# Performance work log

Hardware: AMD Instinct MI355X
Metric: run time of the kernel (lower is better)

The kernel has to match this reference:

```python
import jax, jax.numpy as jnp
import numpy as np

B, TO, C, T = 16, 8, 64, 1024


def setup_inputs() -> dict:
    key = jax.random.key(0)
    kx, kq, kk, kv, ko = jax.random.split(key, 5)
    s = 0.1
    return {
        "x": jax.random.normal(kx, (B, TO, C, T), dtype=jnp.float32),
        "Wq": jax.random.normal(kq, (C, C), dtype=jnp.float32) * s,
        "Wk": jax.random.normal(kk, (C, C), dtype=jnp.float32) * s,
        "Wv": jax.random.normal(kv, (C, C), dtype=jnp.float32) * s,
        "Wo": jax.random.normal(ko, (C, C), dtype=jnp.float32) * s,
        "scale": jnp.float32(1.0 / np.sqrt(C)),
    }


def reference(x, Wq, Wk, Wv, Wo, scale):
    b, to, c, t = x.shape
    xr = x.reshape(b * to, c, t)            # [N, C, T]
    # 1x1 conv1d (no bias) == channel-mixing matmul with weight [out_c, in_c]
    q = jnp.einsum('oc,bct->bot', Wq, xr)
    k = jnp.einsum('oc,bct->bot', Wk, xr)
    v = jnp.einsum('oc,bct->bot', Wv, xr)
    # attention over the time axis: scores [N, T, T]
    scores = jnp.einsum('bct,bcs->bts', q, k) * scale
    w = jax.nn.softmax(scores, axis=-1)
    out = jnp.einsum('bts,bcs->bct', w, v)  # [N, C, T]
    out = jnp.einsum('oc,bct->bot', Wo, out)
    out = out + xr
    return out.reshape(b, to, c, t)
```

## Files before the change

kernel.cpp:

```cpp
#include <hip/hip_runtime.h>
#include <hip/hip_bf16.h>

typedef __hip_bfloat16 bf16;
typedef __attribute__((ext_vector_type(8))) short short8;
typedef __attribute__((ext_vector_type(4))) short short4v;
typedef __attribute__((ext_vector_type(4))) float f32x4;
typedef __attribute__((ext_vector_type(4))) unsigned uint4v;

#define NB 128
#define CC 64
#define TT 1024

#if __has_builtin(__builtin_amdgcn_exp2f)
#define EXP2(x) __builtin_amdgcn_exp2f(x)
#else
#define EXP2(x) exp2f(x)
#endif

__device__ __forceinline__ unsigned rnd_u(float f) {
  return __builtin_bit_cast(unsigned, f) + 0x8000u;
}
__device__ __forceinline__ short f2bfs_fast(float f) {
  return (short)(rnd_u(f) >> 16);
}
__device__ __forceinline__ unsigned packbf2(unsigned uhi, unsigned ulo) {
  return __builtin_amdgcn_perm(uhi, ulo, 0x07060302);
}
__device__ __forceinline__ short4v pack4(float a, float b, float c, float d) {
  unsigned pd[2] = { packbf2(rnd_u(b), rnd_u(a)), packbf2(rnd_u(d), rnd_u(c)) };
  return *(const short4v*)pd;
}

__device__ __forceinline__ f32x4 mfma32(short8 a, short8 b, f32x4 c) {
  return __builtin_amdgcn_mfma_f32_16x16x32_bf16(a, b, c, 0, 0, 0);
}

__global__ __launch_bounds__(256) void wcvt(
    const float* __restrict__ Wq, const float* __restrict__ Wk,
    const float* __restrict__ Wv, const float* __restrict__ Wo,
    const float* __restrict__ scale_p, bf16* __restrict__ wb)
{
  const int i = blockIdx.x * 256 + threadIdx.x;
  float f;
  if      (i <  4096) f = Wq[i] * (*scale_p) * 1.44269504089f;
  else if (i <  8192) f = Wk[i - 4096];
  else if (i < 12288) f = Wv[i - 8192];
  else {
    const int ii = i - 12288;
    const int o  = ii >> 6;
    const int cp = ii & 63;
    const int u  = cp >> 5, q4 = (cp >> 3) & 3, j = cp & 7;
    const int c  = (2 * u + (j >> 2)) * 16 + q4 * 4 + (j & 3);
    f = Wo[o * 64 + c];
  }
  wb[i] = __float2bfloat16(f);
}

__global__ __launch_bounds__(256) void qkv_mfma(
    const float* __restrict__ x, const bf16* __restrict__ wb,
    bf16* __restrict__ qt, bf16* __restrict__ kt, bf16* __restrict__ v)
{
  __shared__ short xs[64 * 72];
  __shared__ short ys[64 * 72];

  const int n  = blockIdx.y;
  const int t0 = blockIdx.x * 64;
  const int tid = threadIdx.x;
  const int w  = tid >> 6, il = tid & 15, q4 = (tid & 63) >> 4;
  const size_t nbase = (size_t)n * (CC * TT);

  {
    const int tc = tid & 15;
    const int c0 = (tid >> 4) * 4;
    float fe[4][4];
    #pragma unroll
    for (int j = 0; j < 4; j++) {
      float4 fj = *(const float4*)&x[nbase + (size_t)(c0 + j) * TT + t0 + tc * 4];
      fe[j][0] = fj.x; fe[j][1] = fj.y; fe[j][2] = fj.z; fe[j][3] = fj.w;
    }
    #pragma unroll
    for (int e = 0; e < 4; e++)
      *(short4v*)&xs[(tc * 4 + e) * 72 + c0] = pack4(fe[0][e], fe[1][e], fe[2][e], fe[3][e]);
  }
  __syncthreads();

  short8 xa[2];
  #pragma unroll
  for (int kk = 0; kk < 2; kk++)
    xa[kk] = *(const short8*)&xs[(w * 16 + il) * 72 + kk * 32 + q4 * 8];

  const bf16* wq = wb;
  const bf16* wk = wb + 4096;
  const bf16* wv = wb + 8192;

  f32x4 aq[4], ak[4], av[4];
  #pragma unroll
  for (int i = 0; i < 4; i++) {
    aq[i] = (f32x4){0.f,0.f,0.f,0.f};
    ak[i] = (f32x4){0.f,0.f,0.f,0.f};
    av[i] = (f32x4){0.f,0.f,0.f,0.f};
  }

  #pragma unroll
  for (int kk = 0; kk < 2; kk++) {
    #pragma unroll
    for (int ot = 0; ot < 4; ot++) {
      const int ridx = (ot * 16 + il) * 64 + kk * 32 + q4 * 8;
      short8 bq = *(const short8*)&wq[ridx];
      short8 bk = *(const short8*)&wk[ridx];
      short8 bv = *(const short8*)&wv[ridx];
      aq[ot] = mfma32(xa[kk], bq, aq[ot]);
      ak[ot] = mfma32(xa[kk], bk, ak[ot]);
      av[ot] = mfma32(bv, xa[kk], av[ot]);
    }
  }

  const int rr = tid >> 2;
  const int sg = (tid & 3) * 8;

  __syncthreads();
  #pragma unroll
  for (int ot = 0; ot < 4; ot++)
    #pragma unroll
    for (int r = 0; r < 4; r++)
      ys[(w * 16 + q4 * 4 + r) * 72 + ot * 16 + il] = f2bfs_fast(aq[ot][r]);
  __syncthreads();
  *(short8*)&qt[nbase + (size_t)(t0 + rr) * 64 + sg]      = *(const short8*)&ys[rr * 72 + sg];
  *(short8*)&qt[nbase + (size_t)(t0 + rr) * 64 + sg + 32] = *(const short8*)&ys[rr * 72 + sg + 32];

  __syncthreads();
  #pragma unroll
  for (int ot = 0; ot < 4; ot++)
    #pragma unroll
    for (int r = 0; r < 4; r++)
      ys[(w * 16 + q4 * 4 + r) * 72 + ot * 16 + il] = f2bfs_fast(ak[ot][r]);
  __syncthreads();
  *(short8*)&kt[nbase + (size_t)(t0 + rr) * 64 + sg]      = *(const short8*)&ys[rr * 72 + sg];
  *(short8*)&kt[nbase + (size_t)(t0 + rr) * 64 + sg + 32] = *(const short8*)&ys[rr * 72 + sg + 32];

  __syncthreads();
  #pragma unroll
  for (int ot = 0; ot < 4; ot++)
    #pragma unroll
    for (int r = 0; r < 4; r++)
      ys[(ot * 16 + q4 * 4 + r) * 72 + (il >> 2) * 16 + w * 4 + (il & 3)] =
          f2bfs_fast(av[ot][r]);
  __syncthreads();
  *(short8*)&v[nbase + (size_t)rr * TT + t0 + sg]      = *(const short8*)&ys[rr * 72 + sg];
  *(short8*)&v[nbase + (size_t)rr * TT + t0 + sg + 32] = *(const short8*)&ys[rr * 72 + sg + 32];
}

__global__ __launch_bounds__(256, 4) void attn_flash(
    const bf16* __restrict__ qt, const bf16* __restrict__ kt,
    const bf16* __restrict__ v,  const bf16* __restrict__ wob,
    const float* __restrict__ x, float* __restrict__ out)
{
  __shared__ float obuf[64 * 132];
  short* ks = (short*)obuf;
  short* vs = ks + 64 * 72;

  const int bid = blockIdx.x;
  const int n   = bid & 127;
  const int qt0 = (bid >> 7) * 128;
  const int tid = threadIdx.x;
  const int w   = tid >> 6;
  const int il  = tid & 15;
  const int q4  = (tid & 63) >> 4;
  const size_t nbase = (size_t)n * (CC * TT);

  const int srow0 = tid >> 3, scol = (tid & 7) * 8;
  const int srow1 = srow0 + 32;

  short8 qb[2][2];
  #pragma unroll
  for (int mt = 0; mt < 2; mt++)
    #pragma unroll
    for (int kk = 0; kk < 2; kk++)
      qb[mt][kk] = *(const short8*)&qt[nbase +
          (size_t)(qt0 + w * 32 + mt * 16 + il) * 64 + kk * 32 + q4 * 8];

  const short8 ones8 = { 0x3F80, 0x3F80, 0x3F80, 0x3F80,
                         0x3F80, 0x3F80, 0x3F80, 0x3F80 };

  f32x4 oaccT[2][4];
  f32x4 lacc[2];
  #pragma unroll
  for (int mt = 0; mt < 2; mt++) {
    lacc[mt] = (f32x4){0.f, 0.f, 0.f, 0.f};
    #pragma unroll
    for (int ct = 0; ct < 4; ct++) oaccT[mt][ct] = (f32x4){0.f, 0.f, 0.f, 0.f};
  }

  short8 kreg0 = *(const short8*)&kt[nbase + (size_t)srow0 * 64 + scol];
  short8 kreg1 = *(const short8*)&kt[nbase + (size_t)srow1 * 64 + scol];
  short8 vreg0 = *(const short8*)&v[nbase + (size_t)srow0 * TT + scol];
  short8 vreg1 = *(const short8*)&v[nbase + (size_t)srow1 * TT + scol];

  #pragma unroll 1
  for (int st = 0; st < 16; st++) {
    __syncthreads();
    *(short8*)&ks[srow0 * 72 + scol] = kreg0;
    *(short8*)&ks[srow1 * 72 + scol] = kreg1;
    *(short8*)&vs[srow0 * 72 + scol] = vreg0;
    *(short8*)&vs[srow1 * 72 + scol] = vreg1;
    if (st < 15) {
      const int s1 = (st + 1) * 64;
      kreg0 = *(const short8*)&kt[nbase + (size_t)(s1 + srow0) * 64 + scol];
      kreg1 = *(const short8*)&kt[nbase + (size_t)(s1 + srow1) * 64 + scol];
      vreg0 = *(const short8*)&v[nbase + (size_t)srow0 * TT + s1 + scol];
      vreg1 = *(const short8*)&v[nbase + (size_t)srow1 * TT + s1 + scol];
    }
    __syncthreads();

    uint4v pq[2][2];
    #pragma unroll
    for (int st2 = 0; st2 < 4; st2++) {
      short8 ka0 = *(const short8*)&ks[(st2 * 16 + il) * 72 + q4 * 8];
      short8 ka1 = *(const short8*)&ks[(st2 * 16 + il) * 72 + 32 + q4 * 8];
      #pragma unroll
      for (int mt = 0; mt < 2; mt++) {
        f32x4 sT = (f32x4){0.f, 0.f, 0.f, 0.f};
        sT = mfma32(ka0, qb[mt][0], sT);
        sT = mfma32(ka1, qb[mt][1], sT);
        float p0 = EXP2(sT[0]), p1 = EXP2(sT[1]), p2 = EXP2(sT[2]), p3 = EXP2(sT[3]);
        pq[mt][st2 >> 1][(st2 & 1) * 2]     = packbf2(rnd_u(p1), rnd_u(p0));
        pq[mt][st2 >> 1][(st2 & 1) * 2 + 1] = packbf2(rnd_u(p3), rnd_u(p2));
      }
    }
    short8 pb[2][2];
    #pragma unroll
    for (int mt = 0; mt < 2; mt++)
      #pragma unroll
      for (int u = 0; u < 2; u++) {
        pb[mt][u] = __builtin_bit_cast(short8, pq[mt][u]);
        lacc[mt] = mfma32(ones8, pb[mt][u], lacc[mt]);
      }

    #pragma unroll
    for (int ct = 0; ct < 4; ct++) {
      short8 h0 = *(const short8*)&vs[(ct * 16 + il) * 72 + q4 * 16];
      short8 h1 = *(const short8*)&vs[(ct * 16 + il) * 72 + q4 * 16 + 8];
      #pragma unroll
      for (int mt = 0; mt < 2; mt++) {
        oaccT[mt][ct] = mfma32(h0, pb[mt][0], oaccT[mt][ct]);
        oaccT[mt][ct] = mfma32(h1, pb[mt][1], oaccT[mt][ct]);
      }
    }
  }

  float linv[2];
  #pragma unroll
  for (int mt = 0; mt < 2; mt++) linv[mt] = 1.f / lacc[mt][0];

  uint4v obq[2][2];
  #pragma unroll
  for (int mt = 0; mt < 2; mt++)
    #pragma unroll
    for (int ct = 0; ct < 4; ct++) {
      float a = oaccT[mt][ct][0] * linv[mt], b = oaccT[mt][ct][1] * linv[mt];
      float c = oaccT[mt][ct][2] * linv[mt], d = oaccT[mt][ct][3] * linv[mt];
      obq[mt][ct >> 1][(ct & 1) * 2]     = packbf2(rnd_u(b), rnd_u(a));
      obq[mt][ct >> 1][(ct & 1) * 2 + 1] = packbf2(rnd_u(d), rnd_u(c));
    }
  short8 ob8[2][2];
  #pragma unroll
  for (int mt = 0; mt < 2; mt++)
    #pragma unroll
    for (int u = 0; u < 2; u++)
      ob8[mt][u] = __builtin_bit_cast(short8, obq[mt][u]);

  __syncthreads();

  #pragma unroll
  for (int ot = 0; ot < 4; ot++) {
    short8 wa0 = *(const short8*)&wob[(ot * 16 + il) * 64 + q4 * 8];
    short8 wa1 = *(const short8*)&wob[(ot * 16 + il) * 64 + 32 + q4 * 8];
    #pragma unroll
    for (int mt = 0; mt < 2; mt++) {
      f32x4 res = (f32x4){0.f, 0.f, 0.f, 0.f};
      res = mfma32(wa0, ob8[mt][0], res);
      res = mfma32(wa1, ob8[mt][1], res);
      #pragma unroll
      for (int r = 0; r < 4; r++)
        obuf[(ot * 16 + q4 * 4 + r) * 132 + w * 32 + mt * 16 + il] = res[r];
    }
  }
  __syncthreads();

  const int orow = tid >> 3;
  const int ocb  = (tid & 7) * 4;
  #pragma unroll
  for (int half = 0; half < 2; half++) {
    const int row = orow + half * 32;
    #pragma unroll
    for (int k = 0; k < 4; k++) {
      const int col = ocb + k * 32;
      float4 val = *(const float4*)&obuf[row * 132 + col];
      const size_t idx = nbase + (size_t)row * TT + qt0 + col;
      float4 xv = *(const float4*)&x[idx];
      val.x += xv.x; val.y += xv.y; val.z += xv.z; val.w += xv.w;
      *(float4*)&out[idx] = val;
    }
  }
}

extern "C" void kernel_launch(void* const* d_in, const int* in_sizes, int n_in,
                              void* d_out, int out_size, void* d_ws, size_t ws_size,
                              hipStream_t stream) {
  const float* x     = (const float*)d_in[0];
  const float* Wq    = (const float*)d_in[1];
  const float* Wk    = (const float*)d_in[2];
  const float* Wv    = (const float*)d_in[3];
  const float* Wo    = (const float*)d_in[4];
  const float* scale = (const float*)d_in[5];
  float* out = (float*)d_out;

  const size_t elems = (size_t)NB * CC * TT;
  bf16* wb  = (bf16*)d_ws;
  bf16* qtb = wb + 16384;
  bf16* ktb = qtb + elems;
  bf16* vv  = ktb + elems;

  wcvt<<<64, 256, 0, stream>>>(Wq, Wk, Wv, Wo, scale, wb);
  qkv_mfma<<<dim3(TT / 64, NB), 256, 0, stream>>>(x, wb, qtb, ktb, vv);
  attn_flash<<<dim3(NB * (TT / 128)), 256, 0, stream>>>(qtb, ktb, vv, wb + 12288, x, out);
}
```

Measured before the change: 158.3 us.

## Fold Wq/Wk and Wo/Wv products and attend directly on x

Precomputes M = Wk^T Wq (with scale and log2e folded in) and W2 = Wo Wv on device, so scores become x^T M x and the output projection absorbs V. The attention kernel now loads fp32 x tiles for keys and values and converts them to bf16 in registers. This removes the QKV projection kernel and its bf16 Q/K/V round trip through global memory. The cost is reading fp32 x (twice the bytes of bf16) for every key/value tile in each block, plus bf16 rounding of the fused weight matrices.

```diff
diff --git a/kernel.cpp b/kernel.cpp
--- a/kernel.cpp
+++ b/kernel.cpp
@@ -20,9 +20,6 @@
 __device__ __forceinline__ unsigned rnd_u(float f) {
   return __builtin_bit_cast(unsigned, f) + 0x8000u;
 }
-__device__ __forceinline__ short f2bfs_fast(float f) {
-  return (short)(rnd_u(f) >> 16);
-}
 __device__ __forceinline__ unsigned packbf2(unsigned uhi, unsigned ulo) {
   return __builtin_amdgcn_perm(uhi, ulo, 0x07060302);
 }
@@ -35,127 +32,36 @@
   return __builtin_amdgcn_mfma_f32_16x16x32_bf16(a, b, c, 0, 0, 0);
 }
 
-__global__ __launch_bounds__(256) void wcvt(
+__global__ __launch_bounds__(256) void wprep(
     const float* __restrict__ Wq, const float* __restrict__ Wk,
     const float* __restrict__ Wv, const float* __restrict__ Wo,
-    const float* __restrict__ scale_p, bf16* __restrict__ wb)
+    const float* __restrict__ scale_p, bf16* __restrict__ wmw)
 {
-  const int i = blockIdx.x * 256 + threadIdx.x;
-  float f;
-  if      (i <  4096) f = Wq[i] * (*scale_p) * 1.44269504089f;
-  else if (i <  8192) f = Wk[i - 4096];
-  else if (i < 12288) f = Wv[i - 8192];
-  else {
-    const int ii = i - 12288;
-    const int o  = ii >> 6;
-    const int cp = ii & 63;
-    const int u  = cp >> 5, q4 = (cp >> 3) & 3, j = cp & 7;
-    const int c  = (2 * u + (j >> 2)) * 16 + q4 * 4 + (j & 3);
-    f = Wo[o * 64 + c];
-  }
-  wb[i] = __float2bfloat16(f);
-}
-
-__global__ __launch_bounds__(256) void qkv_mfma(
-    const float* __restrict__ x, const bf16* __restrict__ wb,
-    bf16* __restrict__ qt, bf16* __restrict__ kt, bf16* __restrict__ v)
-{
-  __shared__ short xs[64 * 72];
-  __shared__ short ys[64 * 72];
-
-  const int n  = blockIdx.y;
-  const int t0 = blockIdx.x * 64;
-  const int tid = threadIdx.x;
-  const int w  = tid >> 6, il = tid & 15, q4 = (tid & 63) >> 4;
-  const size_t nbase = (size_t)n * (CC * TT);
-
-  {
-    const int tc = tid & 15;
-    const int c0 = (tid >> 4) * 4;
-    float fe[4][4];
-    #pragma unroll
-    for (int j = 0; j < 4; j++) {
-      float4 fj = *(const float4*)&x[nbase + (size_t)(c0 + j) * TT + t0 + tc * 4];
-      fe[j][0] = fj.x; fe[j][1] = fj.y; fe[j][2] = fj.z; fe[j][3] = fj.w;
-    }
-    #pragma unroll
-    for (int e = 0; e < 4; e++)
-      *(short4v*)&xs[(tc * 4 + e) * 72 + c0] = pack4(fe[0][e], fe[1][e], fe[2][e], fe[3][e]);
-  }
-  __syncthreads();
-
-  short8 xa[2];
-  #pragma unroll
-  for (int kk = 0; kk < 2; kk++)
-    xa[kk] = *(const short8*)&xs[(w * 16 + il) * 72 + kk * 32 + q4 * 8];
-
-  const bf16* wq = wb;
-  const bf16* wk = wb + 4096;
-  const bf16* wv = wb + 8192;
-
-  f32x4 aq[4], ak[4], av[4];
-  #pragma unroll
-  for (int i = 0; i < 4; i++) {
-    aq[i] = (f32x4){0.f,0.f,0.f,0.f};
-    ak[i] = (f32x4){0.f,0.f,0.f,0.f};
-    av[i] = (f32x4){0.f,0.f,0.f,0.f};
-  }
-
-  #pragma unroll
-  for (int kk = 0; kk < 2; kk++) {
-    #pragma unroll
-    for (int ot = 0; ot < 4; ot++) {
-      const int ridx = (ot * 16 + il) * 64 + kk * 32 + q4 * 8;
-      short8 bq = *(const short8*)&wq[ridx];
-      short8 bk = *(const short8*)&wk[ridx];
-      short8 bv = *(const short8*)&wv[ridx];
-      aq[ot] = mfma32(xa[kk], bq, aq[ot]);
-      ak[ot] = mfma32(xa[kk], bk, ak[ot]);
-      av[ot] = mfma32(bv, xa[kk], av[ot]);
-    }
-  }
-
-  const int rr = tid >> 2;
-  const int sg = (tid & 3) * 8;
-
-  __syncthreads();
-  #pragma unroll
-  for (int ot = 0; ot < 4; ot++)
-    #pragma unroll
-    for (int r = 0; r < 4; r++)
-      ys[(w * 16 + q4 * 4 + r) * 72 + ot * 16 + il] = f2bfs_fast(aq[ot][r]);
-  __syncthreads();
-  *(short8*)&qt[nbase + (size_t)(t0 + rr) * 64 + sg]      = *(const short8*)&ys[rr * 72 + sg];
-  *(short8*)&qt[nbase + (size_t)(t0 + rr) * 64 + sg + 32] = *(const short8*)&ys[rr * 72 + sg + 32];
-
-  __syncthreads();
-  #pragma unroll
-  for (int ot = 0; ot < 4; ot++)
-    #pragma unroll
-    for (int r = 0; r < 4; r++)
-      ys[(w * 16 + q4 * 4 + r) * 72 + ot * 16 + il] = f2bfs_fast(ak[ot][r]);
-  __syncthreads();
-  *(short8*)&kt[nbase + (size_t)(t0 + rr) * 64 + sg]      = *(const short8*)&ys[rr * 72 + sg];
-  *(short8*)&kt[nbase + (size_t)(t0 + rr) * 64 + sg + 32] = *(const short8*)&ys[rr * 72 + sg + 32];
-
-  __syncthreads();
-  #pragma unroll
-  for (int ot = 0; ot < 4; ot++)
-    #pragma unroll
-    for (int r = 0; r < 4; r++)
-      ys[(ot * 16 + q4 * 4 + r) * 72 + (il >> 2) * 16 + w * 4 + (il & 3)] =
-          f2bfs_fast(av[ot][r]);
-  __syncthreads();
-  *(short8*)&v[nbase + (size_t)rr * TT + t0 + sg]      = *(const short8*)&ys[rr * 72 + sg];
-  *(short8*)&v[nbase + (size_t)rr * TT + t0 + sg + 32] = *(const short8*)&ys[rr * 72 + sg + 32];
-}
-
-__global__ __launch_bounds__(256, 4) void attn_flash(
-    const bf16* __restrict__ qt, const bf16* __restrict__ kt,
-    const bf16* __restrict__ v,  const bf16* __restrict__ wob,
+  const int g = blockIdx.x * 256 + threadIdx.x;
+  float acc = 0.f;
+  if (g < 4096) {
+    const int a = g >> 6, b = g & 63;
+    #pragma unroll 8
+    for (int c = 0; c < 64; c++) acc += Wk[c * 64 + a] * Wq[c * 64 + b];
+    acc *= (*scale_p) * 1.44269504089f;
+    wmw[g] = __float2bfloat16(acc);
+  } else {
+    const int ii = g - 4096;
+    const int o = ii >> 6, cp = ii & 63;
+    const int u = cp >> 5, q4 = (cp >> 3) & 3, j = cp & 7;
+    const int a = (2 * u + (j >> 2)) * 16 + q4 * 4 + (j & 3);
+    #pragma unroll 8
+    for (int c = 0; c < 64; c++) acc += Wo[o * 64 + c] * Wv[c * 64 + a];
+    wmw[g] = __float2bfloat16(acc);
+  }
+}
+
+__global__ __launch_bounds__(256, 4) void attn_fused(
+    const bf16* __restrict__ wm, const bf16* __restrict__ w2,
     const float* __restrict__ x, float* __restrict__ out)
 {
   __shared__ float obuf[64 * 132];
+  short* xq = (short*)obuf;
   short* ks = (short*)obuf;
   short* vs = ks + 64 * 72;
 
@@ -168,16 +74,54 @@
   const int q4  = (tid & 63) >> 4;
   const size_t nbase = (size_t)n * (CC * TT);
 
-  const int srow0 = tid >> 3, scol = (tid & 7) * 8;
-  const int srow1 = srow0 + 32;
-
-  short8 qb[2][2];
+  const int tc = tid & 15;
+  const int c0 = (tid >> 4) * 4;
+
+  #pragma unroll
+  for (int half = 0; half < 2; half++) {
+    float fe[4][4];
+    #pragma unroll
+    for (int j = 0; j < 4; j++) {
+      float4 fj = *(const float4*)&x[nbase + (size_t)(c0 + j) * TT + qt0 + half * 64 + tc * 4];
+      fe[j][0] = fj.x; fe[j][1] = fj.y; fe[j][2] = fj.z; fe[j][3] = fj.w;
+    }
+    #pragma unroll
+    for (int e = 0; e < 4; e++)
+      *(short4v*)&xq[(half * 64 + tc * 4 + e) * 72 + c0] =
+          pack4(fe[0][e], fe[1][e], fe[2][e], fe[3][e]);
+  }
+  __syncthreads();
+
+  f32x4 yacc[4][2];
+  #pragma unroll
+  for (int at = 0; at < 4; at++)
+    #pragma unroll
+    for (int mt = 0; mt < 2; mt++) yacc[at][mt] = (f32x4){0.f, 0.f, 0.f, 0.f};
+  #pragma unroll
+  for (int kk = 0; kk < 2; kk++) {
+    short8 xb0 = *(const short8*)&xq[(w * 32 + il) * 72 + kk * 32 + q4 * 8];
+    short8 xb1 = *(const short8*)&xq[(w * 32 + 16 + il) * 72 + kk * 32 + q4 * 8];
+    #pragma unroll
+    for (int at = 0; at < 4; at++) {
+      short8 ma = *(const short8*)&wm[(at * 16 + il) * 64 + kk * 32 + q4 * 8];
+      yacc[at][0] = mfma32(ma, xb0, yacc[at][0]);
+      yacc[at][1] = mfma32(ma, xb1, yacc[at][1]);
+    }
+  }
+  __syncthreads();
+  #pragma unroll
+  for (int at = 0; at < 4; at++)
+    #pragma unroll
+    for (int mt = 0; mt < 2; mt++)
+      *(short4v*)&xq[(w * 32 + mt * 16 + il) * 72 + at * 16 + q4 * 4] =
+          pack4(yacc[at][mt][0], yacc[at][mt][1], yacc[at][mt][2], yacc[at][mt][3]);
+  __syncthreads();
+  short8 yb[2][2];
   #pragma unroll
   for (int mt = 0; mt < 2; mt++)
     #pragma unroll
     for (int kk = 0; kk < 2; kk++)
-      qb[mt][kk] = *(const short8*)&qt[nbase +
-          (size_t)(qt0 + w * 32 + mt * 16 + il) * 64 + kk * 32 + q4 * 8];
+      yb[mt][kk] = *(const short8*)&xq[(w * 32 + mt * 16 + il) * 72 + kk * 32 + q4 * 8];
 
   const short8 ones8 = { 0x3F80, 0x3F80, 0x3F80, 0x3F80,
                          0x3F80, 0x3F80, 0x3F80, 0x3F80 };
@@ -191,24 +135,30 @@
     for (int ct = 0; ct < 4; ct++) oaccT[mt][ct] = (f32x4){0.f, 0.f, 0.f, 0.f};
   }
 
-  short8 kreg0 = *(const short8*)&kt[nbase + (size_t)srow0 * 64 + scol];
-  short8 kreg1 = *(const short8*)&kt[nbase + (size_t)srow1 * 64 + scol];
-  short8 vreg0 = *(const short8*)&v[nbase + (size_t)srow0 * TT + scol];
-  short8 vreg1 = *(const short8*)&v[nbase + (size_t)srow1 * TT + scol];
+  float fe[4][4];
+  #pragma unroll
+  for (int j = 0; j < 4; j++) {
+    float4 fj = *(const float4*)&x[nbase + (size_t)(c0 + j) * TT + tc * 4];
+    fe[j][0] = fj.x; fe[j][1] = fj.y; fe[j][2] = fj.z; fe[j][3] = fj.w;
+  }
 
   #pragma unroll 1
   for (int st = 0; st < 16; st++) {
     __syncthreads();
-    *(short8*)&ks[srow0 * 72 + scol] = kreg0;
-    *(short8*)&ks[srow1 * 72 + scol] = kreg1;
-    *(short8*)&vs[srow0 * 72 + scol] = vreg0;
-    *(short8*)&vs[srow1 * 72 + scol] = vreg1;
+    #pragma unroll
+    for (int e = 0; e < 4; e++)
+      *(short4v*)&ks[(tc * 4 + e) * 72 + c0] = pack4(fe[0][e], fe[1][e], fe[2][e], fe[3][e]);
+    #pragma unroll
+    for (int j = 0; j < 4; j++)
+      *(short4v*)&vs[(c0 + j) * 72 + (tc & 3) * 16 + (tc >> 2) * 4] =
+          pack4(fe[j][0], fe[j][1], fe[j][2], fe[j][3]);
     if (st < 15) {
       const int s1 = (st + 1) * 64;
-      kreg0 = *(const short8*)&kt[nbase + (size_t)(s1 + srow0) * 64 + scol];
-      kreg1 = *(const short8*)&kt[nbase + (size_t)(s1 + srow1) * 64 + scol];
-      vreg0 = *(const short8*)&v[nbase + (size_t)srow0 * TT + s1 + scol];
-      vreg1 = *(const short8*)&v[nbase + (size_t)srow1 * TT + s1 + scol];
+      #pragma unroll
+      for (int j = 0; j < 4; j++) {
+        float4 fj = *(const float4*)&x[nbase + (size_t)(c0 + j) * TT + s1 + tc * 4];
+        fe[j][0] = fj.x; fe[j][1] = fj.y; fe[j][2] = fj.z; fe[j][3] = fj.w;
+      }
     }
     __syncthreads();
 
@@ -220,8 +170,8 @@
       #pragma unroll
       for (int mt = 0; mt < 2; mt++) {
         f32x4 sT = (f32x4){0.f, 0.f, 0.f, 0.f};
-        sT = mfma32(ka0, qb[mt][0], sT);
-        sT = mfma32(ka1, qb[mt][1], sT);
+        sT = mfma32(ka0, yb[mt][0], sT);
+        sT = mfma32(ka1, yb[mt][1], sT);
         float p0 = EXP2(sT[0]), p1 = EXP2(sT[1]), p2 = EXP2(sT[2]), p3 = EXP2(sT[3]);
         pq[mt][st2 >> 1][(st2 & 1) * 2]     = packbf2(rnd_u(p1), rnd_u(p0));
         pq[mt][st2 >> 1][(st2 & 1) * 2 + 1] = packbf2(rnd_u(p3), rnd_u(p2));
@@ -273,8 +223,8 @@
 
   #pragma unroll
   for (int ot = 0; ot < 4; ot++) {
-    short8 wa0 = *(const short8*)&wob[(ot * 16 + il) * 64 + q4 * 8];
-    short8 wa1 = *(const short8*)&wob[(ot * 16 + il) * 64 + 32 + q4 * 8];
+    short8 wa0 = *(const short8*)&w2[(ot * 16 + il) * 64 + q4 * 8];
+    short8 wa1 = *(const short8*)&w2[(ot * 16 + il) * 64 + 32 + q4 * 8];
     #pragma unroll
     for (int mt = 0; mt < 2; mt++) {
       f32x4 res = (f32x4){0.f, 0.f, 0.f, 0.f};
@@ -315,13 +265,8 @@
   const float* scale = (const float*)d_in[5];
   float* out = (float*)d_out;
 
-  const size_t elems = (size_t)NB * CC * TT;
-  bf16* wb  = (bf16*)d_ws;
-  bf16* qtb = wb + 16384;
-  bf16* ktb = qtb + elems;
-  bf16* vv  = ktb + elems;
-
-  wcvt<<<64, 256, 0, stream>>>(Wq, Wk, Wv, Wo, scale, wb);
-  qkv_mfma<<<dim3(TT / 64, NB), 256, 0, stream>>>(x, wb, qtb, ktb, vv);
-  attn_flash<<<dim3(NB * (TT / 128)), 256, 0, stream>>>(qtb, ktb, vv, wb + 12288, x, out);
-}
+  bf16* wmw = (bf16*)d_ws;
+
+  wprep<<<32, 256, 0, stream>>>(Wq, Wk, Wv, Wo, scale, wmw);
+  attn_fused<<<1024, 256, 0, stream>>>(wmw, wmw + 4096, x, out);
+}
```

Result: faster. 140.0 us (-11.6%).
